# Kernel optimization log

Hardware: AMD Instinct MI355X
Metric: run time of the kernel (lower is better)

The kernel has to match this reference:

```python
import jax, jax.numpy as jnp
import numpy as np

N = 100_000
E = 1_600_000
F_IN, D1, D2, D_EMB = 64, 32, 64, 64
NUM_GRAPHS = 16
BN_EPS = 1e-5


def _glorot(key, shape):
    fan_in, fan_out = shape[0], shape[1]
    lim = (6.0 / (fan_in + fan_out)) ** 0.5
    return jax.random.uniform(key, shape, jnp.float32, -lim, lim)


def setup_inputs() -> dict:
    key = jax.random.key(0)
    ks = jax.random.split(key, 12)
    x = jax.random.normal(ks[0], (N, F_IN), jnp.float32)
    edge_index = jax.random.randint(ks[1], (2, E), 0, N, jnp.int64)
    batch = jnp.sort(jax.random.randint(ks[2], (N,), 0, NUM_GRAPHS, jnp.int64))
    return {
        "x": x,
        "edge_index": edge_index,
        "batch": batch,
        "num_graphs": NUM_GRAPHS,
        "num_nodes": N,
        "W1a": _glorot(ks[3], (F_IN, D1)), "b1a": jnp.zeros((D1,), jnp.float32),
        "W1b": _glorot(ks[4], (D1, D2)), "b1b": jnp.zeros((D2,), jnp.float32),
        "g1": jnp.ones((D2,), jnp.float32), "be1": jnp.zeros((D2,), jnp.float32),
        "W2a": _glorot(ks[5], (D2, D2)), "b2a": jnp.zeros((D2,), jnp.float32),
        "W2b": _glorot(ks[6], (D2, D_EMB)), "b2b": jnp.zeros((D_EMB,), jnp.float32),
        "g2": jnp.ones((D_EMB,), jnp.float32), "be2": jnp.zeros((D_EMB,), jnp.float32),
    }


def _batchnorm_train(h, gamma, beta):
    mean = jnp.mean(h, axis=0)
    var = jnp.mean(jnp.square(h - mean), axis=0)  # biased var, as torch BN uses for normalization
    return (h - mean) * jax.lax.rsqrt(var + BN_EPS) * gamma + beta


def _gin_aggregate(x, src, dst, valid, n_nodes):
    # sum_{j in N(i)} x_j over valid edges only (masked scatter-add)
    msg = x[src] * valid[:, None]  # [E, D]
    return jax.ops.segment_sum(msg, dst, num_segments=n_nodes)


def reference(x, edge_index, batch, num_graphs, num_nodes,
              W1a, b1a, W1b, b1b, g1, be1,
              W2a, b2a, W2b, b2b, g2, be2):
    n_edges = edge_index.shape[1]
    per = n_edges // num_graphs
    # edge_mask: per-edge threshold g * num_nodes / num_graphs applied to both rows
    thresh = jnp.repeat(jnp.arange(num_graphs), per).astype(jnp.float32) * (num_nodes / num_graphs)
    valid = jnp.all(edge_index.astype(jnp.float32) - thresh[None, :] >= 0.0, axis=0)
    valid = valid.astype(x.dtype)
    src, dst = edge_index[0], edge_index[1]

    # GINConv 1 (eps=0): nn1(x + aggr)
    h = x + _gin_aggregate(x, src, dst, valid, num_nodes)
    h = jax.nn.relu(h @ W1a + b1a) @ W1b + b1b
    h = jax.nn.relu(h)
    h = _batchnorm_train(h, g1, be1)

    # GINConv 2
    h = h + _gin_aggregate(h, src, dst, valid, num_nodes)
    h = jax.nn.relu(h @ W2a + b2a) @ W2b + b2b
    h = jax.nn.relu(h)
    h = _batchnorm_train(h, g2, be2)

    # global_mean_pool
    sums = jax.ops.segment_sum(h, batch, num_segments=num_graphs)
    counts = jax.ops.segment_sum(jnp.ones((h.shape[0],), h.dtype), batch, num_segments=num_graphs)
    return sums / jnp.maximum(counts, 1.0)[:, None]
```

## Files before the change

kernel.cpp:

```cpp
#include <hip/hip_runtime.h>
#include <hip/hip_fp16.h>

#define NG 16
#define D 64
#define SLOT 32
#define INP 68
#define NPB 64

union HF4 { float4 f4; __half2 h2[4]; };
union HF2 { float2 f2; __half2 h2[2]; };

__device__ __forceinline__ float2 f2fma(float2 a, float2 b, float2 c) {
  return make_float2(fmaf(a.x, b.x, c.x), fmaf(a.y, b.y, c.y));
}
__device__ __forceinline__ float2 f2add(float2 a, float2 b) {
  return make_float2(a.x + b.x, a.y + b.y);
}

__global__ void prep_kernel(const float* __restrict__ x,
                            float2* __restrict__ xh, int n4,
                            float4* __restrict__ xz, float4* __restrict__ hz,
                            const int* __restrict__ ei,
                            int* __restrict__ fill, int* __restrict__ col,
                            int E, int per, int tmul) {
  int t = blockIdx.x * 256 + threadIdx.x;
  if (blockIdx.x == 0 && threadIdx.x < 16) {
    float4 z = make_float4(0.f, 0.f, 0.f, 0.f);
    if (threadIdx.x < 8) xz[threadIdx.x] = z;
    else hz[threadIdx.x - 8] = z;
  }
  if (t < n4) {
    float4 v = ((const float4*)x)[t];
    HF2 u;
    u.h2[0] = __floats2half2_rn(v.x, v.y);
    u.h2[1] = __floats2half2_rn(v.z, v.w);
    xh[t] = u.f2;
  }
  if (t < E) {
    int src = ei[t];
    int dst = ei[E + t];
    int thr = (t / per) * tmul;
    if (src >= thr && dst >= thr) {
      int k = atomicAdd(&fill[dst], 1);
      if (k < SLOT) col[dst * SLOT + k] = src;
    }
  }
}

__device__ __forceinline__ void tree_reduce_2x32(float* s_in, int tid) {
#pragma unroll
  for (int s = 16; s >= 1; s >>= 1) {
    if (tid < 32 * s) {
      int h = tid / (16 * s);
      int r = (tid / 16) % s;
      int qq = tid & 15;
      float4* a = (float4*)&s_in[(h * 32 + r) * INP + qq * 4];
      const float4 b = *(const float4*)&s_in[(h * 32 + r + s) * INP + qq * 4];
      a->x += b.x; a->y += b.y; a->z += b.z; a->w += b.w;
    }
    __syncthreads();
  }
}

template <int MID, bool FOLD_BN, int EPI>
__global__ __launch_bounds__(512, 2) void fused_layer_kernel(
    const float4* __restrict__ feat4,
    const int* __restrict__ col, const int* __restrict__ deg,
    const float* __restrict__ bn_sum, const float* __restrict__ bn_sq,
    const float* __restrict__ bn_gamma, const float* __restrict__ bn_beta,
    float invN,
    const float* __restrict__ Wa, const float* __restrict__ ba,
    const float* __restrict__ Wb, const float* __restrict__ bb,
    float2* __restrict__ out2,
    const int* __restrict__ batch,
    float* __restrict__ st_sum,
    float* __restrict__ st_sq,
    float* __restrict__ cnt,
    int N) {
  __shared__ float s_in[NPB * INP];
  __shared__ __half s_Wa[D * MID];
  __shared__ __half s_Wb[MID * D];
  __shared__ float s_bna[FOLD_BN ? D : 1];
  __shared__ float s_bnb[FOLD_BN ? D : 1];
  __shared__ int s_cnt[2];

  int tid = threadIdx.x;

  {
    const float4* wa4 = (const float4*)Wa;
    const float4* wb4 = (const float4*)Wb;
    __half2* sa2 = (__half2*)s_Wa;
    __half2* sb2 = (__half2*)s_Wb;
    constexpr int NW = D * MID / 4;
#pragma unroll
    for (int i = tid; i < NW; i += 512) {
      float4 a = wa4[i];
      float4 b = wb4[i];
      sa2[2 * i + 0] = __floats2half2_rn(a.x, a.y);
      sa2[2 * i + 1] = __floats2half2_rn(a.z, a.w);
      sb2[2 * i + 0] = __floats2half2_rn(b.x, b.y);
      sb2[2 * i + 1] = __floats2half2_rn(b.z, b.w);
    }
  }
  if (FOLD_BN && tid < D) {
    float mean = bn_sum[tid] * invN;
    float var = bn_sq[tid] * invN - mean * mean;
    float av = bn_gamma[tid] * rsqrtf(var + 1e-5f);
    s_bna[tid] = av;
    s_bnb[tid] = bn_beta[tid] - mean * av;
  }
  if (EPI == 2 && tid < 2) s_cnt[tid] = 0;
  __syncthreads();

  int base = blockIdx.x * NPB;

  {
    int slot = tid >> 3;
    int q8 = tid & 7;
    int node = base + slot;
    if (node < N) {
      int d = min(deg[node], SLOT);
      const int* cl = col + node * SLOT;
      float2 acc[4];
      {
        HF4 s; s.f4 = feat4[(size_t)node * 8 + q8];
#pragma unroll
        for (int i = 0; i < 4; i++) acc[i] = __half22float2(s.h2[i]);
      }
      int dpad = (d + 15) & ~15;
      for (int j = 0; j < dpad; j += 16) {
        int4 sa = *(const int4*)(cl + j);
        int4 sb = *(const int4*)(cl + j + 4);
        int4 sc = *(const int4*)(cl + j + 8);
        int4 sd = *(const int4*)(cl + j + 12);
        int idx[16];
        idx[0]  = (j + 0  < d) ? sa.x : N;  idx[1]  = (j + 1  < d) ? sa.y : N;
        idx[2]  = (j + 2  < d) ? sa.z : N;  idx[3]  = (j + 3  < d) ? sa.w : N;
        idx[4]  = (j + 4  < d) ? sb.x : N;  idx[5]  = (j + 5  < d) ? sb.y : N;
        idx[6]  = (j + 6  < d) ? sb.z : N;  idx[7]  = (j + 7  < d) ? sb.w : N;
        idx[8]  = (j + 8  < d) ? sc.x : N;  idx[9]  = (j + 9  < d) ? sc.y : N;
        idx[10] = (j + 10 < d) ? sc.z : N;  idx[11] = (j + 11 < d) ? sc.w : N;
        idx[12] = (j + 12 < d) ? sd.x : N;  idx[13] = (j + 13 < d) ? sd.y : N;
        idx[14] = (j + 14 < d) ? sd.z : N;  idx[15] = (j + 15 < d) ? sd.w : N;
        HF4 u[16];
#pragma unroll
        for (int i = 0; i < 16; i++) u[i].f4 = feat4[(size_t)idx[i] * 8 + q8];
#pragma unroll
        for (int i = 0; i < 16; i++) {
#pragma unroll
          for (int c = 0; c < 4; c++)
            acc[c] = f2add(acc[c], __half22float2(u[i].h2[c]));
        }
      }
      if (FOLD_BN) {
        float dp = (float)(d + 1);
        int c0 = q8 * 8;
#pragma unroll
        for (int c = 0; c < 4; c++) {
          float2 a2 = *(const float2*)&s_bna[c0 + 2 * c];
          float2 b2 = *(const float2*)&s_bnb[c0 + 2 * c];
          acc[c] = f2fma(a2, acc[c], make_float2(dp * b2.x, dp * b2.y));
        }
      }
      *(float4*)&s_in[slot * INP + q8 * 8] =
          make_float4(acc[0].x, acc[0].y, acc[1].x, acc[1].y);
      *(float4*)&s_in[slot * INP + q8 * 8 + 4] =
          make_float4(acc[2].x, acc[2].y, acc[3].x, acc[3].y);
    }
  }
  __syncthreads();

  int q = tid & 15;
  int r2 = tid >> 4;
  int n0 = 2 * r2, n1 = n0 + 1;
  int node0 = base + n0, node1 = base + n1;
  constexpr int C1 = MID / 16;
  constexpr int C2 = C1 / 2;
  float4 o0, o1;
  {
    float2 acc0[C2], acc1[C2];
#pragma unroll
    for (int u = 0; u < C2; u++) {
      acc0[u] = *(const float2*)&ba[q * C1 + 2 * u];
      acc1[u] = acc0[u];
    }
#pragma unroll 4
    for (int j = 0; j < D; j++) {
      float2 v0 = make_float2(s_in[n0 * INP + j], s_in[n0 * INP + j]);
      float2 v1 = make_float2(s_in[n1 * INP + j], s_in[n1 * INP + j]);
      if constexpr (C1 == 2) {
        float2 w = __half22float2(((const __half2*)s_Wa)[j * 16 + q]);
        acc0[0] = f2fma(v0, w, acc0[0]);
        acc1[0] = f2fma(v1, w, acc1[0]);
      } else {
        HF2 u; u.f2 = ((const float2*)s_Wa)[j * 16 + q];
        float2 wA = __half22float2(u.h2[0]);
        float2 wB = __half22float2(u.h2[1]);
        acc0[0] = f2fma(v0, wA, acc0[0]);
        acc0[1] = f2fma(v0, wB, acc0[1]);
        acc1[0] = f2fma(v1, wA, acc1[0]);
        acc1[1] = f2fma(v1, wB, acc1[1]);
      }
    }
#pragma unroll
    for (int u = 0; u < C2; u++) {
      acc0[u].x = fmaxf(acc0[u].x, 0.f); acc0[u].y = fmaxf(acc0[u].y, 0.f);
      acc1[u].x = fmaxf(acc1[u].x, 0.f); acc1[u].y = fmaxf(acc1[u].y, 0.f);
    }

    float2 o0a = *(const float2*)&bb[q * 4];
    float2 o0b = *(const float2*)&bb[q * 4 + 2];
    float2 o1a = o0a, o1b = o0b;
#pragma unroll 8
    for (int k = 0; k < MID; k++) {
      float s0 = ((k % C1) & 1) ? acc0[(k % C1) >> 1].y : acc0[(k % C1) >> 1].x;
      float s1 = ((k % C1) & 1) ? acc1[(k % C1) >> 1].y : acc1[(k % C1) >> 1].x;
      float m0 = __shfl(s0, k / C1, 16);
      float m1 = __shfl(s1, k / C1, 16);
      HF2 u; u.f2 = ((const float2*)s_Wb)[k * 16 + q];
      float2 wA = __half22float2(u.h2[0]);
      float2 wB = __half22float2(u.h2[1]);
      float2 m0f = make_float2(m0, m0);
      float2 m1f = make_float2(m1, m1);
      o0a = f2fma(m0f, wA, o0a); o0b = f2fma(m0f, wB, o0b);
      o1a = f2fma(m1f, wA, o1a); o1b = f2fma(m1f, wB, o1b);
    }
    o0 = make_float4(fmaxf(o0a.x, 0.f), fmaxf(o0a.y, 0.f),
                     fmaxf(o0b.x, 0.f), fmaxf(o0b.y, 0.f));
    o1 = make_float4(fmaxf(o1a.x, 0.f), fmaxf(o1a.y, 0.f),
                     fmaxf(o1b.x, 0.f), fmaxf(o1b.y, 0.f));
    if (EPI == 1) {
      if (node0 < N) {
        HF2 u;
        u.h2[0] = __floats2half2_rn(o0.x, o0.y);
        u.h2[1] = __floats2half2_rn(o0.z, o0.w);
        out2[(size_t)node0 * 16 + q] = u.f2;
      }
      if (node1 < N) {
        HF2 u;
        u.h2[0] = __floats2half2_rn(o1.x, o1.y);
        u.h2[1] = __floats2half2_rn(o1.z, o1.w);
        out2[(size_t)node1 * 16 + q] = u.f2;
      }
    }
    if (node0 >= N) o0 = make_float4(0.f, 0.f, 0.f, 0.f);
    if (node1 >= N) o1 = make_float4(0.f, 0.f, 0.f, 0.f);
  }

  if (EPI == 1) {
    __syncthreads();
    *(float4*)&s_in[r2 * INP + q * 4] =
        make_float4(o0.x + o1.x, o0.y + o1.y, o0.z + o1.z, o0.w + o1.w);
    *(float4*)&s_in[(32 + r2) * INP + q * 4] =
        make_float4(o0.x * o0.x + o1.x * o1.x, o0.y * o0.y + o1.y * o1.y,
                    o0.z * o0.z + o1.z * o1.z, o0.w * o0.w + o1.w * o1.w);
    __syncthreads();
    tree_reduce_2x32(s_in, tid);
    if (tid < D) {
      atomicAdd(&st_sum[tid], s_in[tid]);
      atomicAdd(&st_sq[tid], s_in[32 * INP + tid]);
    }
  }

  if (EPI == 2) {
    int b0 = (node0 < N) ? batch[node0] : -1;
    int b1 = (node1 < N) ? batch[node1] : -1;
    int g_lo = batch[base];
    int g_hi = batch[min(base + NPB - 1, N - 1)];

    __syncthreads();
    if (q == 0) {
      atomicAdd(&s_cnt[0], (b0 == g_lo ? 1 : 0) + (b1 == g_lo ? 1 : 0));
      if (g_hi != g_lo)
        atomicAdd(&s_cnt[1], (b0 == g_hi ? 1 : 0) + (b1 == g_hi ? 1 : 0));
    }

    float w0 = (b0 == g_lo) ? 1.f : 0.f;
    float w1 = (b1 == g_lo) ? 1.f : 0.f;
    *(float4*)&s_in[r2 * INP + q * 4] =
        make_float4(w0 * o0.x + w1 * o1.x, w0 * o0.y + w1 * o1.y,
                    w0 * o0.z + w1 * o1.z, w0 * o0.w + w1 * o1.w);
    *(float4*)&s_in[(32 + r2) * INP + q * 4] =
        make_float4(o0.x * o0.x + o1.x * o1.x, o0.y * o0.y + o1.y * o1.y,
                    o0.z * o0.z + o1.z * o1.z, o0.w * o0.w + o1.w * o1.w);
    __syncthreads();
    tree_reduce_2x32(s_in, tid);
    if (tid < D) {
      atomicAdd(&st_sum[g_lo * D + tid], s_in[tid]);
      atomicAdd(&st_sq[tid], s_in[32 * INP + tid]);
    }
    if (tid == 0) atomicAdd(&cnt[g_lo], (float)s_cnt[0]);

    if (g_hi != g_lo) {
      __syncthreads();
      float u0 = (b0 == g_hi) ? 1.f : 0.f;
      float u1 = (b1 == g_hi) ? 1.f : 0.f;
      *(float4*)&s_in[r2 * INP + q * 4] =
          make_float4(u0 * o0.x + u1 * o1.x, u0 * o0.y + u1 * o1.y,
                      u0 * o0.z + u1 * o1.z, u0 * o0.w + u1 * o1.w);
      *(float4*)&s_in[(32 + r2) * INP + q * 4] = make_float4(0.f, 0.f, 0.f, 0.f);
      __syncthreads();
      tree_reduce_2x32(s_in, tid);
      if (tid < D) atomicAdd(&st_sum[g_hi * D + tid], s_in[tid]);
      if (tid == 0) atomicAdd(&cnt[g_hi], (float)s_cnt[1]);
    }
  }
}

__global__ void final_kernel(const float* __restrict__ pool,
                             const float* __restrict__ cnt,
                             const float* __restrict__ sq,
                             const float* __restrict__ gamma,
                             const float* __restrict__ beta,
                             float invN, float* __restrict__ out) {
  int c = threadIdx.x;
  float s = 0.f;
#pragma unroll
  for (int g = 0; g < NG; g++) s += pool[g * D + c];
  float mean = s * invN;
  float var = sq[c] * invN - mean * mean;
  float a = gamma[c] * rsqrtf(var + 1e-5f);
  float b = beta[c] - mean * a;
#pragma unroll
  for (int g = 0; g < NG; g++) {
    float n = cnt[g];
    out[g * D + c] = (a * pool[g * D + c] + n * b) / fmaxf(n, 1.f);
  }
}

extern "C" void kernel_launch(void* const* d_in, const int* in_sizes, int n_in,
                              void* d_out, int out_size, void* d_ws, size_t ws_size,
                              hipStream_t stream) {
  const float* x   = (const float*)d_in[0];
  const int* ei    = (const int*)d_in[1];
  const int* batch = (const int*)d_in[2];
  const float* W1a = (const float*)d_in[5];
  const float* b1a = (const float*)d_in[6];
  const float* W1b = (const float*)d_in[7];
  const float* b1b = (const float*)d_in[8];
  const float* g1  = (const float*)d_in[9];
  const float* be1 = (const float*)d_in[10];
  const float* W2a = (const float*)d_in[11];
  const float* b2a = (const float*)d_in[12];
  const float* W2b = (const float*)d_in[13];
  const float* b2b = (const float*)d_in[14];
  const float* g2  = (const float*)d_in[15];
  const float* be2 = (const float*)d_in[16];

  int N = in_sizes[0] / D;
  int E = in_sizes[1] / 2;
  int per = E / NG;
  int tmul = N / NG;
  float invN = 1.f / (float)N;

  float* ws = (float*)d_ws;
  size_t ndh = (size_t)(N + 1) * D / 2;
  float* h1h = ws;
  float* xh  = ws + ndh;
  int*   col = (int*)(ws + 2 * ndh);
  float* stats = ws + 2 * ndh + (size_t)N * SLOT;
  float* sum1 = stats;
  float* sq1  = stats + 64;
  float* pool = stats + 128;
  float* cnt  = stats + 128 + NG * D;
  float* sq2  = stats + 144 + NG * D;
  int*   fill = (int*)(stats + 208 + NG * D);

  hipMemsetAsync(stats, 0, (208 + NG * D + N) * sizeof(float), stream);

  int n4 = N * D / 4;
  int pgrid = (max(n4, E) + 255) / 256;
  prep_kernel<<<pgrid, 256, 0, stream>>>(
      x, (float2*)xh, n4,
      (float4*)(xh + (size_t)N * D / 2),
      (float4*)(h1h + (size_t)N * D / 2),
      ei, fill, col, E, per, tmul);

  int fblocks = (N + NPB - 1) / NPB;

  fused_layer_kernel<32, false, 1><<<fblocks, 512, 0, stream>>>(
      (const float4*)xh, col, fill, nullptr, nullptr, nullptr, nullptr, invN,
      W1a, b1a, W1b, b1b, (float2*)h1h, nullptr, sum1, sq1, nullptr, N);

  fused_layer_kernel<64, true, 2><<<fblocks, 512, 0, stream>>>(
      (const float4*)h1h, col, fill, sum1, sq1, g1, be1, invN,
      W2a, b2a, W2b, b2b, nullptr, batch, pool, sq2, cnt, N);

  final_kernel<<<1, 64, 0, stream>>>(pool, cnt, sq2, g2, be2, invN, (float*)d_out);
}
```

Measured before the change: 254.1 us.

## Use MFMA f16 matrix cores for fused GIN MLP with wave-level reductions

Replaces the scalar FMA two-layer MLP with MFMA 16x16x16 f16 instructions, staging aggregated features in shared memory as half precision and prepacking weights into the MFMA operand layout. The block size grows to 128 nodes, and each thread aggregates two nodes. The shared-memory tree reduction for batch-norm statistics and pooling is replaced by shuffle-xor reductions inside each wave plus one cross-wave pass. The intent is to cut ALU time and barrier count in the MLP and epilogue. The cost is lower precision, since the aggregated inputs are rounded to f16 before the matmul, plus larger per-block work that may reduce occupancy.

```diff
diff --git a/kernel.cpp b/kernel.cpp
--- a/kernel.cpp
+++ b/kernel.cpp
@@ -4,11 +4,14 @@
 #define NG 16
 #define D 64
 #define SLOT 32
-#define INP 68
-#define NPB 64
+#define NPB 128
+#define INH 72
 
 union HF4 { float4 f4; __half2 h2[4]; };
 union HF2 { float2 f2; __half2 h2[2]; };
+
+typedef _Float16 half4_t __attribute__((ext_vector_type(4)));
+typedef float float4_t __attribute__((ext_vector_type(4)));
 
 __device__ __forceinline__ float2 f2fma(float2 a, float2 b, float2 c) {
   return make_float2(fmaf(a.x, b.x, c.x), fmaf(a.y, b.y, c.y));
@@ -44,21 +47,6 @@
       int k = atomicAdd(&fill[dst], 1);
       if (k < SLOT) col[dst * SLOT + k] = src;
     }
-  }
-}
-
-__device__ __forceinline__ void tree_reduce_2x32(float* s_in, int tid) {
-#pragma unroll
-  for (int s = 16; s >= 1; s >>= 1) {
-    if (tid < 32 * s) {
-      int h = tid / (16 * s);
-      int r = (tid / 16) % s;
-      int qq = tid & 15;
-      float4* a = (float4*)&s_in[(h * 32 + r) * INP + qq * 4];
-      const float4 b = *(const float4*)&s_in[(h * 32 + r + s) * INP + qq * 4];
-      a->x += b.x; a->y += b.y; a->z += b.z; a->w += b.w;
-    }
-    __syncthreads();
   }
 }
 
@@ -77,31 +65,47 @@
     float* __restrict__ st_sq,
     float* __restrict__ cnt,
     int N) {
-  __shared__ float s_in[NPB * INP];
-  __shared__ __half s_Wa[D * MID];
-  __shared__ __half s_Wb[MID * D];
+  constexpr int CT = MID / 16;
+
+  __shared__ __align__(16) __half s_h[NPB * INH];
+  __shared__ __align__(16) __half s_wa[MID * 64];
+  __shared__ __align__(16) __half s_wb[64 * MID];
+  __shared__ __align__(16) float s_ba[MID];
+  __shared__ __align__(16) float s_bb[D];
   __shared__ float s_bna[FOLD_BN ? D : 1];
   __shared__ float s_bnb[FOLD_BN ? D : 1];
   __shared__ int s_cnt[2];
 
   int tid = threadIdx.x;
+  int base = blockIdx.x * NPB;
 
   {
-    const float4* wa4 = (const float4*)Wa;
-    const float4* wb4 = (const float4*)Wb;
-    __half2* sa2 = (__half2*)s_Wa;
-    __half2* sb2 = (__half2*)s_Wb;
-    constexpr int NW = D * MID / 4;
-#pragma unroll
-    for (int i = tid; i < NW; i += 512) {
-      float4 a = wa4[i];
-      float4 b = wb4[i];
-      sa2[2 * i + 0] = __floats2half2_rn(a.x, a.y);
-      sa2[2 * i + 1] = __floats2half2_rn(a.z, a.w);
-      sb2[2 * i + 0] = __floats2half2_rn(b.x, b.y);
-      sb2[2 * i + 1] = __floats2half2_rn(b.z, b.w);
-    }
-  }
+    constexpr int WA_SLOTS = MID * 16;
+    constexpr int WB_SLOTS = MID * 16;
+    for (int g = tid; g < WA_SLOTS + WB_SLOTS; g += 512) {
+      half4_t v;
+      if (g < WA_SLOTS) {
+        int l = g & 63, kt = (g >> 6) & 3, ct = g >> 8;
+        int k0 = kt * 16 + ((l >> 4) << 2);
+        int c = ct * 16 + (l & 15);
+#pragma unroll
+        for (int i = 0; i < 4; i++) v[i] = (_Float16)Wa[(k0 + i) * MID + c];
+        *(half4_t*)&s_wa[g * 4] = v;
+      } else {
+        int g2 = g - WA_SLOTS;
+        int l = g2 & 63;
+        int kt = (g2 >> 6) & (CT - 1);
+        int ot = g2 >> (6 + (CT == 4 ? 2 : 1));
+        int k0 = kt * 16 + ((l >> 4) << 2);
+        int o = ot * 16 + (l & 15);
+#pragma unroll
+        for (int i = 0; i < 4; i++) v[i] = (_Float16)Wb[(k0 + i) * D + o];
+        *(half4_t*)&s_wb[g2 * 4] = v;
+      }
+    }
+  }
+  if (tid < MID) s_ba[tid] = ba[tid];
+  if (tid < D) s_bb[tid] = bb[tid];
   if (FOLD_BN && tid < D) {
     float mean = bn_sum[tid] * invN;
     float var = bn_sq[tid] * invN - mean * mean;
@@ -112,197 +116,214 @@
   if (EPI == 2 && tid < 2) s_cnt[tid] = 0;
   __syncthreads();
 
-  int base = blockIdx.x * NPB;
-
   {
-    int slot = tid >> 3;
     int q8 = tid & 7;
-    int node = base + slot;
-    if (node < N) {
-      int d = min(deg[node], SLOT);
-      const int* cl = col + node * SLOT;
+#pragma unroll
+    for (int s0 = 0; s0 < 2; s0++) {
+      int slot = (tid >> 3) + 64 * s0;
+      int node = base + slot;
       float2 acc[4];
-      {
-        HF4 s; s.f4 = feat4[(size_t)node * 8 + q8];
-#pragma unroll
-        for (int i = 0; i < 4; i++) acc[i] = __half22float2(s.h2[i]);
-      }
-      int dpad = (d + 15) & ~15;
-      for (int j = 0; j < dpad; j += 16) {
-        int4 sa = *(const int4*)(cl + j);
-        int4 sb = *(const int4*)(cl + j + 4);
-        int4 sc = *(const int4*)(cl + j + 8);
-        int4 sd = *(const int4*)(cl + j + 12);
-        int idx[16];
-        idx[0]  = (j + 0  < d) ? sa.x : N;  idx[1]  = (j + 1  < d) ? sa.y : N;
-        idx[2]  = (j + 2  < d) ? sa.z : N;  idx[3]  = (j + 3  < d) ? sa.w : N;
-        idx[4]  = (j + 4  < d) ? sb.x : N;  idx[5]  = (j + 5  < d) ? sb.y : N;
-        idx[6]  = (j + 6  < d) ? sb.z : N;  idx[7]  = (j + 7  < d) ? sb.w : N;
-        idx[8]  = (j + 8  < d) ? sc.x : N;  idx[9]  = (j + 9  < d) ? sc.y : N;
-        idx[10] = (j + 10 < d) ? sc.z : N;  idx[11] = (j + 11 < d) ? sc.w : N;
-        idx[12] = (j + 12 < d) ? sd.x : N;  idx[13] = (j + 13 < d) ? sd.y : N;
-        idx[14] = (j + 14 < d) ? sd.z : N;  idx[15] = (j + 15 < d) ? sd.w : N;
-        HF4 u[16];
-#pragma unroll
-        for (int i = 0; i < 16; i++) u[i].f4 = feat4[(size_t)idx[i] * 8 + q8];
-#pragma unroll
-        for (int i = 0; i < 16; i++) {
-#pragma unroll
-          for (int c = 0; c < 4; c++)
-            acc[c] = f2add(acc[c], __half22float2(u[i].h2[c]));
+      if (node < N) {
+        int d = min(deg[node], SLOT);
+        const int* cl = col + node * SLOT;
+        {
+          HF4 s; s.f4 = feat4[(size_t)node * 8 + q8];
+#pragma unroll
+          for (int i = 0; i < 4; i++) acc[i] = __half22float2(s.h2[i]);
         }
-      }
-      if (FOLD_BN) {
-        float dp = (float)(d + 1);
-        int c0 = q8 * 8;
-#pragma unroll
-        for (int c = 0; c < 4; c++) {
-          float2 a2 = *(const float2*)&s_bna[c0 + 2 * c];
-          float2 b2 = *(const float2*)&s_bnb[c0 + 2 * c];
-          acc[c] = f2fma(a2, acc[c], make_float2(dp * b2.x, dp * b2.y));
+        int dpad = (d + 15) & ~15;
+        for (int j = 0; j < dpad; j += 16) {
+          int4 sa = *(const int4*)(cl + j);
+          int4 sb = *(const int4*)(cl + j + 4);
+          int4 sc = *(const int4*)(cl + j + 8);
+          int4 sd = *(const int4*)(cl + j + 12);
+          int idx[16];
+          idx[0]  = (j + 0  < d) ? sa.x : N;  idx[1]  = (j + 1  < d) ? sa.y : N;
+          idx[2]  = (j + 2  < d) ? sa.z : N;  idx[3]  = (j + 3  < d) ? sa.w : N;
+          idx[4]  = (j + 4  < d) ? sb.x : N;  idx[5]  = (j + 5  < d) ? sb.y : N;
+          idx[6]  = (j + 6  < d) ? sb.z : N;  idx[7]  = (j + 7  < d) ? sb.w : N;
+          idx[8]  = (j + 8  < d) ? sc.x : N;  idx[9]  = (j + 9  < d) ? sc.y : N;
+          idx[10] = (j + 10 < d) ? sc.z : N;  idx[11] = (j + 11 < d) ? sc.w : N;
+          idx[12] = (j + 12 < d) ? sd.x : N;  idx[13] = (j + 13 < d) ? sd.y : N;
+          idx[14] = (j + 14 < d) ? sd.z : N;  idx[15] = (j + 15 < d) ? sd.w : N;
+          HF4 u[16];
+#pragma unroll
+          for (int i = 0; i < 16; i++) u[i].f4 = feat4[(size_t)idx[i] * 8 + q8];
+#pragma unroll
+          for (int i = 0; i < 16; i++) {
+#pragma unroll
+            for (int c = 0; c < 4; c++)
+              acc[c] = f2add(acc[c], __half22float2(u[i].h2[c]));
+          }
         }
-      }
-      *(float4*)&s_in[slot * INP + q8 * 8] =
-          make_float4(acc[0].x, acc[0].y, acc[1].x, acc[1].y);
-      *(float4*)&s_in[slot * INP + q8 * 8 + 4] =
-          make_float4(acc[2].x, acc[2].y, acc[3].x, acc[3].y);
+        if (FOLD_BN) {
+          float dp = (float)(d + 1);
+          int c0 = q8 * 8;
+#pragma unroll
+          for (int c = 0; c < 4; c++) {
+            float2 a2 = *(const float2*)&s_bna[c0 + 2 * c];
+            float2 b2 = *(const float2*)&s_bnb[c0 + 2 * c];
+            acc[c] = f2fma(a2, acc[c], make_float2(dp * b2.x, dp * b2.y));
+          }
+        }
+      } else {
+#pragma unroll
+        for (int i = 0; i < 4; i++) acc[i] = make_float2(0.f, 0.f);
+      }
+      HF4 o;
+#pragma unroll
+      for (int c = 0; c < 4; c++)
+        o.h2[c] = __floats2half2_rn(acc[c].x, acc[c].y);
+      *(float4*)&s_h[slot * INH + q8 * 8] = o.f4;
     }
   }
   __syncthreads();
 
-  int q = tid & 15;
-  int r2 = tid >> 4;
-  int n0 = 2 * r2, n1 = n0 + 1;
-  int node0 = base + n0, node1 = base + n1;
-  constexpr int C1 = MID / 16;
-  constexpr int C2 = C1 / 2;
-  float4 o0, o1;
-  {
-    float2 acc0[C2], acc1[C2];
-#pragma unroll
-    for (int u = 0; u < C2; u++) {
-      acc0[u] = *(const float2*)&ba[q * C1 + 2 * u];
-      acc1[u] = acc0[u];
-    }
-#pragma unroll 4
-    for (int j = 0; j < D; j++) {
-      float2 v0 = make_float2(s_in[n0 * INP + j], s_in[n0 * INP + j]);
-      float2 v1 = make_float2(s_in[n1 * INP + j], s_in[n1 * INP + j]);
-      if constexpr (C1 == 2) {
-        float2 w = __half22float2(((const __half2*)s_Wa)[j * 16 + q]);
-        acc0[0] = f2fma(v0, w, acc0[0]);
-        acc1[0] = f2fma(v1, w, acc1[0]);
-      } else {
-        HF2 u; u.f2 = ((const float2*)s_Wa)[j * 16 + q];
-        float2 wA = __half22float2(u.h2[0]);
-        float2 wB = __half22float2(u.h2[1]);
-        acc0[0] = f2fma(v0, wA, acc0[0]);
-        acc0[1] = f2fma(v0, wB, acc0[1]);
-        acc1[0] = f2fma(v1, wA, acc1[0]);
-        acc1[1] = f2fma(v1, wB, acc1[1]);
-      }
-    }
-#pragma unroll
-    for (int u = 0; u < C2; u++) {
-      acc0[u].x = fmaxf(acc0[u].x, 0.f); acc0[u].y = fmaxf(acc0[u].y, 0.f);
-      acc1[u].x = fmaxf(acc1[u].x, 0.f); acc1[u].y = fmaxf(acc1[u].y, 0.f);
-    }
-
-    float2 o0a = *(const float2*)&bb[q * 4];
-    float2 o0b = *(const float2*)&bb[q * 4 + 2];
-    float2 o1a = o0a, o1b = o0b;
-#pragma unroll 8
-    for (int k = 0; k < MID; k++) {
-      float s0 = ((k % C1) & 1) ? acc0[(k % C1) >> 1].y : acc0[(k % C1) >> 1].x;
-      float s1 = ((k % C1) & 1) ? acc1[(k % C1) >> 1].y : acc1[(k % C1) >> 1].x;
-      float m0 = __shfl(s0, k / C1, 16);
-      float m1 = __shfl(s1, k / C1, 16);
-      HF2 u; u.f2 = ((const float2*)s_Wb)[k * 16 + q];
-      float2 wA = __half22float2(u.h2[0]);
-      float2 wB = __half22float2(u.h2[1]);
-      float2 m0f = make_float2(m0, m0);
-      float2 m1f = make_float2(m1, m1);
-      o0a = f2fma(m0f, wA, o0a); o0b = f2fma(m0f, wB, o0b);
-      o1a = f2fma(m1f, wA, o1a); o1b = f2fma(m1f, wB, o1b);
-    }
-    o0 = make_float4(fmaxf(o0a.x, 0.f), fmaxf(o0a.y, 0.f),
-                     fmaxf(o0b.x, 0.f), fmaxf(o0b.y, 0.f));
-    o1 = make_float4(fmaxf(o1a.x, 0.f), fmaxf(o1a.y, 0.f),
-                     fmaxf(o1b.x, 0.f), fmaxf(o1b.y, 0.f));
-    if (EPI == 1) {
-      if (node0 < N) {
+  int w = tid >> 6;
+  int l = tid & 63;
+  int lg = l >> 4;
+  int ln = l & 15;
+  int nodeB = base + w * 16 + ln;
+
+  half4_t hb[4];
+#pragma unroll
+  for (int kt = 0; kt < 4; kt++)
+    hb[kt] = *(const half4_t*)&s_h[(w * 16 + ln) * INH + kt * 16 + lg * 4];
+
+  float4_t c1[CT];
+#pragma unroll
+  for (int ct = 0; ct < CT; ct++) {
+    c1[ct] = *(const float4_t*)&s_ba[ct * 16 + lg * 4];
+#pragma unroll
+    for (int kt = 0; kt < 4; kt++) {
+      half4_t a = *(const half4_t*)&s_wa[((ct * 4 + kt) * 64 + l) * 4];
+      c1[ct] = __builtin_amdgcn_mfma_f32_16x16x16f16(a, hb[kt], c1[ct], 0, 0, 0);
+    }
+  }
+  half4_t mb[CT];
+#pragma unroll
+  for (int ct = 0; ct < CT; ct++) {
+#pragma unroll
+    for (int r = 0; r < 4; r++) mb[ct][r] = (_Float16)fmaxf(c1[ct][r], 0.f);
+  }
+  float4_t o4[4];
+#pragma unroll
+  for (int ot = 0; ot < 4; ot++) {
+    o4[ot] = *(const float4_t*)&s_bb[ot * 16 + lg * 4];
+#pragma unroll
+    for (int kt = 0; kt < CT; kt++) {
+      half4_t a = *(const half4_t*)&s_wb[((ot * CT + kt) * 64 + l) * 4];
+      o4[ot] = __builtin_amdgcn_mfma_f32_16x16x16f16(a, mb[kt], o4[ot], 0, 0, 0);
+    }
+#pragma unroll
+    for (int r = 0; r < 4; r++) o4[ot][r] = fmaxf(o4[ot][r], 0.f);
+  }
+
+  float* red = (float*)s_h;
+
+  if (EPI == 1) {
+    bool val = nodeB < N;
+    if (val) {
+#pragma unroll
+      for (int ot = 0; ot < 4; ot++) {
         HF2 u;
-        u.h2[0] = __floats2half2_rn(o0.x, o0.y);
-        u.h2[1] = __floats2half2_rn(o0.z, o0.w);
-        out2[(size_t)node0 * 16 + q] = u.f2;
-      }
-      if (node1 < N) {
-        HF2 u;
-        u.h2[0] = __floats2half2_rn(o1.x, o1.y);
-        u.h2[1] = __floats2half2_rn(o1.z, o1.w);
-        out2[(size_t)node1 * 16 + q] = u.f2;
-      }
-    }
-    if (node0 >= N) o0 = make_float4(0.f, 0.f, 0.f, 0.f);
-    if (node1 >= N) o1 = make_float4(0.f, 0.f, 0.f, 0.f);
-  }
-
-  if (EPI == 1) {
+        u.h2[0] = __floats2half2_rn(o4[ot][0], o4[ot][1]);
+        u.h2[1] = __floats2half2_rn(o4[ot][2], o4[ot][3]);
+        out2[(size_t)nodeB * 16 + ot * 4 + lg] = u.f2;
+      }
+    }
+    float vm = val ? 1.f : 0.f;
+#pragma unroll
+    for (int ot = 0; ot < 4; ot++) {
+      float4_t s, q;
+#pragma unroll
+      for (int r = 0; r < 4; r++) {
+        float x = vm * o4[ot][r];
+        s[r] = x; q[r] = x * o4[ot][r];
+      }
+#pragma unroll
+      for (int m = 1; m < 16; m <<= 1) {
+#pragma unroll
+        for (int r = 0; r < 4; r++) {
+          s[r] += __shfl_xor(s[r], m);
+          q[r] += __shfl_xor(q[r], m);
+        }
+      }
+      if (ln == 0) {
+        *(float4_t*)&red[w * 576 + ot * 16 + lg * 4] = s;
+        *(float4_t*)&red[w * 576 + 64 + ot * 16 + lg * 4] = q;
+      }
+    }
     __syncthreads();
-    *(float4*)&s_in[r2 * INP + q * 4] =
-        make_float4(o0.x + o1.x, o0.y + o1.y, o0.z + o1.z, o0.w + o1.w);
-    *(float4*)&s_in[(32 + r2) * INP + q * 4] =
-        make_float4(o0.x * o0.x + o1.x * o1.x, o0.y * o0.y + o1.y * o1.y,
-                    o0.z * o0.z + o1.z * o1.z, o0.w * o0.w + o1.w * o1.w);
-    __syncthreads();
-    tree_reduce_2x32(s_in, tid);
     if (tid < D) {
-      atomicAdd(&st_sum[tid], s_in[tid]);
-      atomicAdd(&st_sq[tid], s_in[32 * INP + tid]);
+      float s = 0.f, q = 0.f;
+#pragma unroll
+      for (int ww = 0; ww < 8; ww++) {
+        s += red[ww * 576 + tid];
+        q += red[ww * 576 + 64 + tid];
+      }
+      atomicAdd(&st_sum[tid], s);
+      atomicAdd(&st_sq[tid], q);
     }
   }
 
   if (EPI == 2) {
-    int b0 = (node0 < N) ? batch[node0] : -1;
-    int b1 = (node1 < N) ? batch[node1] : -1;
+    bool val = nodeB < N;
+    int bl = val ? batch[nodeB] : -1;
     int g_lo = batch[base];
     int g_hi = batch[min(base + NPB - 1, N - 1)];
-
+    float vm = val ? 1.f : 0.f;
+    float wlo = (bl == g_lo) ? 1.f : 0.f;
+    unsigned long long mlo = __ballot(lg == 0 && bl == g_lo);
+    unsigned long long mhi = __ballot(lg == 0 && val && bl != g_lo);
+    if (l == 0) {
+      atomicAdd(&s_cnt[0], (int)__popcll(mlo));
+      atomicAdd(&s_cnt[1], (int)__popcll(mhi));
+    }
+#pragma unroll
+    for (int ot = 0; ot < 4; ot++) {
+      float4_t sl, st, sq;
+#pragma unroll
+      for (int r = 0; r < 4; r++) {
+        float x = vm * o4[ot][r];
+        sl[r] = wlo * x;
+        st[r] = x;
+        sq[r] = x * o4[ot][r];
+      }
+#pragma unroll
+      for (int m = 1; m < 16; m <<= 1) {
+#pragma unroll
+        for (int r = 0; r < 4; r++) {
+          sl[r] += __shfl_xor(sl[r], m);
+          st[r] += __shfl_xor(st[r], m);
+          sq[r] += __shfl_xor(sq[r], m);
+        }
+      }
+      if (ln == 0) {
+        *(float4_t*)&red[w * 576 + ot * 16 + lg * 4] = sl;
+        float4_t sh;
+#pragma unroll
+        for (int r = 0; r < 4; r++) sh[r] = st[r] - sl[r];
+        *(float4_t*)&red[w * 576 + 64 + ot * 16 + lg * 4] = sh;
+        *(float4_t*)&red[w * 576 + 128 + ot * 16 + lg * 4] = sq;
+      }
+    }
     __syncthreads();
-    if (q == 0) {
-      atomicAdd(&s_cnt[0], (b0 == g_lo ? 1 : 0) + (b1 == g_lo ? 1 : 0));
-      if (g_hi != g_lo)
-        atomicAdd(&s_cnt[1], (b0 == g_hi ? 1 : 0) + (b1 == g_hi ? 1 : 0));
-    }
-
-    float w0 = (b0 == g_lo) ? 1.f : 0.f;
-    float w1 = (b1 == g_lo) ? 1.f : 0.f;
-    *(float4*)&s_in[r2 * INP + q * 4] =
-        make_float4(w0 * o0.x + w1 * o1.x, w0 * o0.y + w1 * o1.y,
-                    w0 * o0.z + w1 * o1.z, w0 * o0.w + w1 * o1.w);
-    *(float4*)&s_in[(32 + r2) * INP + q * 4] =
-        make_float4(o0.x * o0.x + o1.x * o1.x, o0.y * o0.y + o1.y * o1.y,
-                    o0.z * o0.z + o1.z * o1.z, o0.w * o0.w + o1.w * o1.w);
-    __syncthreads();
-    tree_reduce_2x32(s_in, tid);
     if (tid < D) {
-      atomicAdd(&st_sum[g_lo * D + tid], s_in[tid]);
-      atomicAdd(&st_sq[tid], s_in[32 * INP + tid]);
-    }
-    if (tid == 0) atomicAdd(&cnt[g_lo], (float)s_cnt[0]);
-
-    if (g_hi != g_lo) {
-      __syncthreads();
-      float u0 = (b0 == g_hi) ? 1.f : 0.f;
-      float u1 = (b1 == g_hi) ? 1.f : 0.f;
-      *(float4*)&s_in[r2 * INP + q * 4] =
-          make_float4(u0 * o0.x + u1 * o1.x, u0 * o0.y + u1 * o1.y,
-                      u0 * o0.z + u1 * o1.z, u0 * o0.w + u1 * o1.w);
-      *(float4*)&s_in[(32 + r2) * INP + q * 4] = make_float4(0.f, 0.f, 0.f, 0.f);
-      __syncthreads();
-      tree_reduce_2x32(s_in, tid);
-      if (tid < D) atomicAdd(&st_sum[g_hi * D + tid], s_in[tid]);
-      if (tid == 0) atomicAdd(&cnt[g_hi], (float)s_cnt[1]);
+      float sl = 0.f, sh = 0.f, sq = 0.f;
+#pragma unroll
+      for (int ww = 0; ww < 8; ww++) {
+        sl += red[ww * 576 + tid];
+        sh += red[ww * 576 + 64 + tid];
+        sq += red[ww * 576 + 128 + tid];
+      }
+      atomicAdd(&st_sum[g_lo * D + tid], sl);
+      if (g_hi != g_lo) atomicAdd(&st_sum[g_hi * D + tid], sh);
+      atomicAdd(&st_sq[tid], sq);
+    }
+    if (tid == 0) {
+      atomicAdd(&cnt[g_lo], (float)s_cnt[0]);
+      if (g_hi != g_lo) atomicAdd(&cnt[g_hi], (float)s_cnt[1]);
     }
   }
 }
```

After: 222.7 us. 12.4% less time.
